# Kernel optimization log

Hardware: AMD Instinct MI355X
Metric: run time of the kernel (lower is better)

The kernel has to match this reference:

```python
import jax, jax.numpy as jnp
import numpy as np

N = 33554432  # 32M elements, 128 MB fp32

def setup_inputs() -> dict:
    key = jax.random.key(0)
    inp = jax.random.uniform(key, (N,), dtype=jnp.float32)
    return {"inp": inp}

def reference(inp) -> jnp.ndarray:
    # Faithful to the original: exp(x) / sum(exp(inp)) with NO max-subtraction
    # (the torch module computes the unstabilized softmax).
    e = jnp.exp(inp)
    return e / jnp.sum(e)
```

## Files before the change

### kernel.cpp

```cpp
#include <hip/hip_runtime.h>


#define BLOCK 256
#define GRID 2048

typedef float vfloat4 __attribute__((ext_vector_type(4)));

__global__ __launch_bounds__(BLOCK) void softmax_reduce(
    const float* __restrict__ inp, float* __restrict__ partials, int n4) {
  const vfloat4* __restrict__ in4 = (const vfloat4*)inp;
  const int tid = blockIdx.x * BLOCK + threadIdx.x;
  const int stride = gridDim.x * BLOCK;

  float s0 = 0.0f, s1 = 0.0f, s2 = 0.0f, s3 = 0.0f;
  int i = tid;
  for (; i + 3 * stride < n4; i += 4 * stride) {
    vfloat4 a = in4[i];
    vfloat4 b = in4[i + stride];
    vfloat4 c = in4[i + 2 * stride];
    vfloat4 d = in4[i + 3 * stride];
    s0 += __expf(a.x) + __expf(a.y) + __expf(a.z) + __expf(a.w);
    s1 += __expf(b.x) + __expf(b.y) + __expf(b.z) + __expf(b.w);
    s2 += __expf(c.x) + __expf(c.y) + __expf(c.z) + __expf(c.w);
    s3 += __expf(d.x) + __expf(d.y) + __expf(d.z) + __expf(d.w);
  }
  for (; i < n4; i += stride) {
    vfloat4 a = in4[i];
    s0 += __expf(a.x) + __expf(a.y) + __expf(a.z) + __expf(a.w);
  }
  float s = (s0 + s1) + (s2 + s3);

  #pragma unroll
  for (int off = 32; off > 0; off >>= 1)
    s += __shfl_down(s, off, 64);

  __shared__ float wsum[BLOCK / 64];
  if ((threadIdx.x & 63) == 0) wsum[threadIdx.x >> 6] = s;
  __syncthreads();
  if (threadIdx.x == 0)
    partials[blockIdx.x] = wsum[0] + wsum[1] + wsum[2] + wsum[3];
}

__global__ __launch_bounds__(BLOCK) void softmax_scale(
    const float* __restrict__ inp, float* __restrict__ out,
    const float* __restrict__ partials, int n4) {
  float t = 0.0f;
  #pragma unroll
  for (int k = 0; k < GRID / BLOCK; ++k)
    t += partials[k * BLOCK + threadIdx.x];

  #pragma unroll
  for (int off = 32; off > 0; off >>= 1)
    t += __shfl_down(t, off, 64);

  __shared__ float wsum[BLOCK / 64];
  if ((threadIdx.x & 63) == 0) wsum[threadIdx.x >> 6] = t;
  __syncthreads();
  const float r = 1.0f / (wsum[0] + wsum[1] + wsum[2] + wsum[3]);

  const vfloat4* __restrict__ in4 = (const vfloat4*)inp;
  vfloat4* __restrict__ out4 = (vfloat4*)out;
  const int tid = blockIdx.x * BLOCK + threadIdx.x;
  const int stride = gridDim.x * BLOCK;

  int i = tid;
  for (; i + 3 * stride < n4; i += 4 * stride) {
    vfloat4 a = in4[i];
    vfloat4 b = in4[i + stride];
    vfloat4 c = in4[i + 2 * stride];
    vfloat4 d = in4[i + 3 * stride];
    vfloat4 oa, ob, oc, od;
    oa.x = __expf(a.x) * r; oa.y = __expf(a.y) * r;
    oa.z = __expf(a.z) * r; oa.w = __expf(a.w) * r;
    ob.x = __expf(b.x) * r; ob.y = __expf(b.y) * r;
    ob.z = __expf(b.z) * r; ob.w = __expf(b.w) * r;
    oc.x = __expf(c.x) * r; oc.y = __expf(c.y) * r;
    oc.z = __expf(c.z) * r; oc.w = __expf(c.w) * r;
    od.x = __expf(d.x) * r; od.y = __expf(d.y) * r;
    od.z = __expf(d.z) * r; od.w = __expf(d.w) * r;
    __builtin_nontemporal_store(oa, &out4[i]);
    __builtin_nontemporal_store(ob, &out4[i + stride]);
    __builtin_nontemporal_store(oc, &out4[i + 2 * stride]);
    __builtin_nontemporal_store(od, &out4[i + 3 * stride]);
  }
  for (; i < n4; i += stride) {
    vfloat4 a = in4[i];
    vfloat4 oa;
    oa.x = __expf(a.x) * r; oa.y = __expf(a.y) * r;
    oa.z = __expf(a.z) * r; oa.w = __expf(a.w) * r;
    __builtin_nontemporal_store(oa, &out4[i]);
  }
}

extern "C" void kernel_launch(void* const* d_in, const int* in_sizes, int n_in,
                              void* d_out, int out_size, void* d_ws, size_t ws_size,
                              hipStream_t stream) {
  const float* inp = (const float*)d_in[0];
  float* out = (float*)d_out;
  float* partials = (float*)d_ws;
  int n = in_sizes[0];
  int n4 = n >> 2;

  softmax_reduce<<<GRID, BLOCK, 0, stream>>>(inp, partials, n4);
  softmax_scale<<<GRID, BLOCK, 0, stream>>>(inp, out, partials, n4);
}
```

Measured before the change: 248.1 us.

## Fuse reduce and scale kernels with a grid-wide atomic barrier

Merges the two-pass softmax into one persistent kernel with 1024 blocks. Each block writes its partial sum and increments an atomic counter; the last block to arrive reduces the partials, publishes the total and sets a flag, while every block spin-waits on that flag before the scaling pass. This removes a kernel launch boundary and may let the second read of the input hit in cache, but it relies on all 1024 blocks being co-resident (launch bounds set to 4 blocks per SM) and adds a memset plus a spin barrier.

```diff
diff --git a/kernel.cpp b/kernel.cpp
--- a/kernel.cpp
+++ b/kernel.cpp
@@ -2,15 +2,22 @@
 
 
 #define BLOCK 256
-#define GRID 2048
+#define GRID 1024
 
 typedef float vfloat4 __attribute__((ext_vector_type(4)));
 
-__global__ __launch_bounds__(BLOCK) void softmax_reduce(
-    const float* __restrict__ inp, float* __restrict__ partials, int n4) {
+__global__ __launch_bounds__(BLOCK, 4) void softmax_fused(
+    const float* __restrict__ inp, float* __restrict__ out,
+    int* __restrict__ ws_i, float* __restrict__ ws_f, int n4) {
+  int* cnt = ws_i;
+  int* flag = ws_i + 1;
+  float* total = ws_f + 2;
+  float* partials = ws_f + 4;
+
   const vfloat4* __restrict__ in4 = (const vfloat4*)inp;
+  vfloat4* __restrict__ out4 = (vfloat4*)out;
   const int tid = blockIdx.x * BLOCK + threadIdx.x;
-  const int stride = gridDim.x * BLOCK;
+  const int stride = GRID * BLOCK;
 
   float s0 = 0.0f, s1 = 0.0f, s2 = 0.0f, s3 = 0.0f;
   int i = tid;
@@ -35,35 +42,46 @@
     s += __shfl_down(s, off, 64);
 
   __shared__ float wsum[BLOCK / 64];
+  __shared__ int is_last;
+  __shared__ float r_bcast;
   if ((threadIdx.x & 63) == 0) wsum[threadIdx.x >> 6] = s;
   __syncthreads();
-  if (threadIdx.x == 0)
+
+  if (threadIdx.x == 0) {
     partials[blockIdx.x] = wsum[0] + wsum[1] + wsum[2] + wsum[3];
-}
+    __threadfence();
+    int old = atomicAdd(cnt, 1);
+    is_last = (old == GRID - 1);
+  }
+  __syncthreads();
 
-__global__ __launch_bounds__(BLOCK) void softmax_scale(
-    const float* __restrict__ inp, float* __restrict__ out,
-    const float* __restrict__ partials, int n4) {
-  float t = 0.0f;
-  #pragma unroll
-  for (int k = 0; k < GRID / BLOCK; ++k)
-    t += partials[k * BLOCK + threadIdx.x];
+  if (is_last) {
+    float t = 0.0f;
+    #pragma unroll
+    for (int k = 0; k < GRID / BLOCK; ++k)
+      t += __hip_atomic_load(&partials[k * BLOCK + threadIdx.x],
+                             __ATOMIC_RELAXED, __HIP_MEMORY_SCOPE_AGENT);
+    #pragma unroll
+    for (int off = 32; off > 0; off >>= 1)
+      t += __shfl_down(t, off, 64);
+    if ((threadIdx.x & 63) == 0) wsum[threadIdx.x >> 6] = t;
+    __syncthreads();
+    if (threadIdx.x == 0) {
+      *total = wsum[0] + wsum[1] + wsum[2] + wsum[3];
+      __hip_atomic_store(flag, 1, __ATOMIC_RELEASE, __HIP_MEMORY_SCOPE_AGENT);
+    }
+  }
 
-  #pragma unroll
-  for (int off = 32; off > 0; off >>= 1)
-    t += __shfl_down(t, off, 64);
+  if (threadIdx.x == 0) {
+    while (__hip_atomic_load(flag, __ATOMIC_ACQUIRE, __HIP_MEMORY_SCOPE_AGENT) == 0)
+      __builtin_amdgcn_s_sleep(2);
+    float tot = __hip_atomic_load(total, __ATOMIC_RELAXED, __HIP_MEMORY_SCOPE_AGENT);
+    r_bcast = 1.0f / tot;
+  }
+  __syncthreads();
+  const float r = r_bcast;
 
-  __shared__ float wsum[BLOCK / 64];
-  if ((threadIdx.x & 63) == 0) wsum[threadIdx.x >> 6] = t;
-  __syncthreads();
-  const float r = 1.0f / (wsum[0] + wsum[1] + wsum[2] + wsum[3]);
-
-  const vfloat4* __restrict__ in4 = (const vfloat4*)inp;
-  vfloat4* __restrict__ out4 = (vfloat4*)out;
-  const int tid = blockIdx.x * BLOCK + threadIdx.x;
-  const int stride = gridDim.x * BLOCK;
-
-  int i = tid;
+  i = tid;
   for (; i + 3 * stride < n4; i += 4 * stride) {
     vfloat4 a = in4[i];
     vfloat4 b = in4[i + stride];
@@ -97,10 +115,9 @@
                               hipStream_t stream) {
   const float* inp = (const float*)d_in[0];
   float* out = (float*)d_out;
-  float* partials = (float*)d_ws;
   int n = in_sizes[0];
   int n4 = n >> 2;
 
-  softmax_reduce<<<GRID, BLOCK, 0, stream>>>(inp, partials, n4);
-  softmax_scale<<<GRID, BLOCK, 0, stream>>>(inp, out, partials, n4);
+  hipMemsetAsync(d_ws, 0, 8, stream);
+  softmax_fused<<<GRID, BLOCK, 0, stream>>>(inp, out, (int*)d_ws, (float*)d_ws, n4);
 }
```

New measurement: 367.3 us. 48.0% more time.
